# Optimization experiments

Hardware: AMD Instinct MI355X
Metric: run time of the kernel (lower is better)

Reference implementation:

```python
import jax, jax.numpy as jnp
import numpy as np

B = 256        # graph pairs
MAX_SET = 64   # nodes per graph == max_set_size (padding is identity)
E = 512        # edges per graph
D = 128        # node_state_dim == av.filters_3
T = 64         # av.transform_dim
N_PROP = 5
N_TIME = 3
TEMP = 0.1
SINK_ITERS = 20
NG = 2 * B
N = NG * MAX_SET
TOT_E = NG * E


def sinkhorn(log_alpha):
    la = log_alpha / TEMP
    for _ in range(SINK_ITERS):
        la = la - jax.nn.logsumexp(la, axis=2, keepdims=True)
        la = la - jax.nn.logsumexp(la, axis=1, keepdims=True)
    return jnp.exp(la)


def setup_inputs() -> dict:
    key = jax.random.key(0)
    ks = jax.random.split(key, 32)

    def lin(k, i, o):
        return jax.random.normal(k, (i, o), jnp.float32) / np.sqrt(i).astype(np.float32)

    node_features = jax.random.normal(ks[0], (N, 32), jnp.float32)
    edge_features = jax.random.normal(ks[1], (TOT_E, 16), jnp.float32)
    offs = jnp.repeat(jnp.arange(NG, dtype=jnp.int32) * MAX_SET, E)
    from_idx = jax.random.randint(ks[2], (TOT_E,), 0, MAX_SET, jnp.int32) + offs
    to_idx = jax.random.randint(ks[3], (TOT_E,), 0, MAX_SET, jnp.int32) + offs
    return {
        "node_features": node_features, "edge_features": edge_features,
        "from_idx": from_idx, "to_idx": to_idx,
        "node_enc_w": lin(ks[4], 32, D), "node_enc_b": jnp.zeros((D,), jnp.float32),
        "edge_enc_w": lin(ks[5], 16, 64), "edge_enc_b": jnp.zeros((64,), jnp.float32),
        "mw1": lin(ks[6], 2 * D + 64, 2 * D), "mb1": jnp.zeros((2 * D,), jnp.float32),
        "mw2": lin(ks[7], 2 * D, D), "mb2": jnp.zeros((D,), jnp.float32),
        "nw1": lin(ks[8], 2 * D, 2 * D), "nb1": jnp.zeros((2 * D,), jnp.float32),
        "nw2": lin(ks[9], 2 * D, D), "nb2": jnp.zeros((D,), jnp.float32),
        "cw1": lin(ks[10], 2 * D, 2 * D), "cb1": jnp.zeros((2 * D,), jnp.float32),
        "cw2": lin(ks[11], 2 * D, D), "cb2": jnp.zeros((D,), jnp.float32),
        "t1w": lin(ks[12], D, T), "t1b": jnp.zeros((T,), jnp.float32),
        "t2w": lin(ks[13], T, T), "t2b": jnp.zeros((T,), jnp.float32),
    }


def reference(node_features, edge_features, from_idx, to_idx,
              node_enc_w, node_enc_b, edge_enc_w, edge_enc_b,
              mw1, mb1, mw2, mb2, nw1, nb1, nw2, nb2,
              cw1, cb1, cw2, cb2, t1w, t1b, t2w, t2b):
    # Encoder (GMN GraphEncoder: linear maps on raw node/edge features)
    h0 = node_features @ node_enc_w + node_enc_b          # [N, D]
    e0 = edge_features @ edge_enc_w + edge_enc_b          # [TOT_E, 64]
    store = jnp.zeros((N, D * (N_PROP + 1)), h0.dtype)    # node_feature_store
    plan = None
    for _t in range(N_TIME):
        h = h0
        parts = [jnp.zeros((N, D), h0.dtype)]             # slot 0 stays zero
        for p in range(1, N_PROP + 1):
            inter = store[:, (p - 1) * D: p * D]          # time_update_idx == 'k_t'
            comb = jax.nn.relu(jnp.concatenate([h, inter], 1) @ cw1 + cb1) @ cw2 + cb2
            # GraphPropLayer: gather -> message MLP -> segment_sum -> node update MLP
            msg_in = jnp.concatenate([comb[from_idx], comb[to_idx], e0], 1)
            messages = jax.nn.relu(msg_in @ mw1 + mb1) @ mw2 + mb2
            agg = jax.ops.segment_sum(messages, to_idx, num_segments=N)
            h = jax.nn.relu(jnp.concatenate([comb, agg], 1) @ nw1 + nb1) @ nw2 + nb2
            parts.append(h)
        store = jnp.concatenate(parts, 1)                 # [N, D*(K+1)]
        # split into padded query/corpus stacks (all graphs have MAX_SET nodes,
        # so F.pad and the size masks are identity here)
        s = store.reshape(NG, MAX_SET, -1)
        q, c = s[0::2], s[1::2]                           # [B, M, D*(K+1)]
        tq = jax.nn.relu(q[:, :, -D:] @ t1w + t1b) @ t2w + t2b
        tc = jax.nn.relu(c[:, :, -D:] @ t1w + t1b) @ t2w + t2b
        sim = jnp.einsum('bqt,bct->bqc', tq, tc)
        plan = sinkhorn(sim)                              # node transport plan [B,M,M]
        qfc = jnp.einsum('bqc,bcd->bqd', plan, c)
        cfq = jnp.einsum('bqc,bqd->bcd', plan, q)
        inter_feats = jnp.stack([qfc, cfq], 1)[:, :, :, D:].reshape(N, N_PROP * D)
        store = store.at[:, D:].set(inter_feats)
    return plan
```

## Files before the change

### kernel.cpp

```cpp
#include <hip/hip_runtime.h>
#include <hip/hip_bf16.h>

#define NNODES   32768
#define NGROUPS  512
#define EPG      512
#define ND       (32768l*128)

typedef __attribute__((ext_vector_type(4))) float f32x4;
typedef __attribute__((ext_vector_type(8))) short bf16x8;

__device__ __forceinline__ short f2bf(float x) {
  unsigned u = __float_as_uint(x);
  unsigned r = (u + 0x7FFF + ((u >> 16) & 1)) >> 16;
  return (short)r;
}
__device__ __forceinline__ float bf2f(short h) {
  return __uint_as_float(((unsigned)(unsigned short)h) << 16);
}
__device__ __forceinline__ void split3(float x, short* ph, short* pm, short* pl, int idx) {
  short h = f2bf(x); float r1 = x - bf2f(h);
  short m = f2bf(r1); float r2 = r1 - bf2f(m);
  ph[idx] = h; pm[idx] = m; pl[idx] = f2bf(r2);
}

__global__ void k_node_enc(const float* __restrict__ nf, const float* __restrict__ w,
                           const float* __restrict__ b, float* __restrict__ h0) {
  int idx = blockIdx.x * 256 + threadIdx.x;
  int row = idx >> 7, col = idx & 127;
  const float* x = nf + row * 32;
  float acc = b[col];
#pragma unroll
  for (int k = 0; k < 32; ++k) acc = fmaf(x[k], w[k * 128 + col], acc);
  h0[idx] = acc;
}

__global__ void k_prep(const float* __restrict__ eew, const float* __restrict__ eeb,
                       const float* __restrict__ mw1, const float* __restrict__ mb1,
                       const float* __restrict__ mb2, const float* __restrict__ nw1,
                       float* __restrict__ Wfold, float* __restrict__ bfold,
                       float* __restrict__ vbias) {
  const int c = threadIdx.x, b = blockIdx.x;
  if (b < 16) {
    float a = 0.f;
    for (int j = 0; j < 64; ++j) a = fmaf(eew[b * 64 + j], mw1[(256 + j) * 256 + c], a);
    Wfold[b * 256 + c] = a;
  } else if (b == 16) {
    float a = mb1[c];
    for (int j = 0; j < 64; ++j) a = fmaf(eeb[j], mw1[(256 + j) * 256 + c], a);
    bfold[c] = a;
  } else {
    float a = 0.f;
    for (int j = 0; j < 128; ++j) a = fmaf(mb2[j], nw1[(128 + j) * 256 + c], a);
    vbias[c] = a;
  }
}

__global__ void k_wsplit3(const float* __restrict__ W, int C, int Kd,
                          short* __restrict__ th, short* __restrict__ tm,
                          short* __restrict__ tl) {
  const int c = blockIdx.x;
  for (int k = threadIdx.x; k < Kd; k += 256) {
    float w = W[(long)k * C + c];
    split3(w, th, tm, tl, c * 256 + k);
  }
}

__global__ void k_csr(const int* __restrict__ from_idx, const int* __restrict__ to_idx,
                      const float* __restrict__ ef,
                      int* __restrict__ csr_f, int* __restrict__ rp_g,
                      float* __restrict__ efp, int* __restrict__ deg) {
  __shared__ int cnt[64], rps[65];
  __shared__ int tls[EPG], fls[EPG];
  __shared__ short ord[EPG];
  const int g = blockIdx.x, tid = threadIdx.x;
  const int be = g * EPG, bn = g * 64;
  if (tid < 64) cnt[tid] = 0;
  __syncthreads();
  for (int e = tid; e < EPG; e += 256) {
    int t = to_idx[be + e] - bn;
    tls[e] = t;
    fls[e] = from_idx[be + e] - bn;
    atomicAdd(&cnt[t], 1);
  }
  __syncthreads();
  if (tid == 0) {
    int s = 0;
    for (int i = 0; i < 64; ++i) { rps[i] = s; s += cnt[i]; }
    rps[64] = s;
  }
  __syncthreads();
  if (tid < 64) {
    int pos = rps[tid];
    for (int e = 0; e < EPG; ++e)
      if (tls[e] == tid) ord[pos++] = (short)e;
  }
  __syncthreads();
  for (int ec = tid; ec < EPG; ec += 256) {
    const int eo = ord[ec];
    csr_f[be + ec] = fls[eo];
    const float4* src = (const float4*)&ef[(long)(be + eo) * 16];
    float4* dst = (float4*)&efp[(long)(be + ec) * 16];
    dst[0] = src[0]; dst[1] = src[1]; dst[2] = src[2]; dst[3] = src[3];
  }
  if (tid < 65) rp_g[g * 65 + tid] = rps[tid];
  if (tid < 64) deg[bn + tid] = cnt[tid];
}

template<int KTOT, bool DEG, bool SUM2>
__global__ __launch_bounds__(256, 2)
void k_mlp2m(const float* __restrict__ x0, const float* __restrict__ x1,
             const float* __restrict__ x1b,
             const short* __restrict__ W1h, const short* __restrict__ W1m,
             const short* __restrict__ W1l,
             const float* __restrict__ b1, const int* __restrict__ deg,
             const float* __restrict__ vbias,
             const short* __restrict__ W2h, const short* __restrict__ W2m,
             const short* __restrict__ W2l,
             const float* __restrict__ b2, float* __restrict__ out) {
  __shared__ short xh[32 * 264];
  __shared__ short xm[32 * 264];
  __shared__ short xl[32 * 264];
  __shared__ int degs[32];
  const int tid = threadIdx.x;
  const long row0 = (long)blockIdx.x * 32;

  for (int i = tid; i < 32 * 32; i += 256) {
    const int r = i >> 5, q = i & 31;
    float4 v = *(const float4*)&x0[(row0 + r) * 128 + q * 4];
    const int base = r * 264 + q * 4;
    split3(v.x, xh, xm, xl, base + 0);
    split3(v.y, xh, xm, xl, base + 1);
    split3(v.z, xh, xm, xl, base + 2);
    split3(v.w, xh, xm, xl, base + 3);
  }
  if constexpr (KTOT == 256) {
    for (int i = tid; i < 32 * 32; i += 256) {
      const int r = i >> 5, q = i & 31;
      float4 v = *(const float4*)&x1[(row0 + r) * 128 + q * 4];
      if constexpr (SUM2) {
        float4 w = *(const float4*)&x1b[(row0 + r) * 128 + q * 4];
        v.x += w.x; v.y += w.y; v.z += w.z; v.w += w.w;
      }
      const int base = r * 264 + 128 + q * 4;
      split3(v.x, xh, xm, xl, base + 0);
      split3(v.y, xh, xm, xl, base + 1);
      split3(v.z, xh, xm, xl, base + 2);
      split3(v.w, xh, xm, xl, base + 3);
    }
  }
  if constexpr (DEG) { if (tid < 32) degs[tid] = deg[row0 + tid]; }
  __syncthreads();

  const int lane = tid & 63, wid = tid >> 6;
  const int lr = lane & 15;
  const int lk = (lane >> 4) * 8;
  const int rsub = (lane >> 4) * 4;

  f32x4 acc[2][4];
#pragma unroll
  for (int fc = 0; fc < 4; ++fc) {
    const int col = wid * 64 + fc * 16 + lr;
    const float bv = b1[col];
#pragma unroll
    for (int fr = 0; fr < 2; ++fr) acc[fr][fc] = {bv, bv, bv, bv};
    if constexpr (DEG) {
      const float vb = vbias[col];
#pragma unroll
      for (int fr = 0; fr < 2; ++fr)
#pragma unroll
        for (int r = 0; r < 4; ++r)
          acc[fr][fc][r] += (float)degs[fr * 16 + rsub + r] * vb;
    }
  }

  for (int ks = 0; ks < KTOT / 32; ++ks) {
    const int k0 = ks * 32 + lk;
    bf16x8 ah[2], am[2], al[2];
#pragma unroll
    for (int fr = 0; fr < 2; ++fr) {
      const int ab = (fr * 16 + lr) * 264 + k0;
      ah[fr] = *(const bf16x8*)&xh[ab];
      am[fr] = *(const bf16x8*)&xm[ab];
      al[fr] = *(const bf16x8*)&xl[ab];
    }
#pragma unroll
    for (int fc = 0; fc < 4; ++fc) {
      const long wrow = (long)(wid * 64 + fc * 16 + lr) * 256 + k0;
      const bf16x8 bh = *(const bf16x8*)&W1h[wrow];
      const bf16x8 bm = *(const bf16x8*)&W1m[wrow];
      const bf16x8 bl = *(const bf16x8*)&W1l[wrow];
#pragma unroll
      for (int fr = 0; fr < 2; ++fr) {
        acc[fr][fc] = __builtin_amdgcn_mfma_f32_16x16x32_bf16(ah[fr], bh, acc[fr][fc], 0, 0, 0);
        acc[fr][fc] = __builtin_amdgcn_mfma_f32_16x16x32_bf16(ah[fr], bm, acc[fr][fc], 0, 0, 0);
        acc[fr][fc] = __builtin_amdgcn_mfma_f32_16x16x32_bf16(am[fr], bh, acc[fr][fc], 0, 0, 0);
        acc[fr][fc] = __builtin_amdgcn_mfma_f32_16x16x32_bf16(ah[fr], bl, acc[fr][fc], 0, 0, 0);
        acc[fr][fc] = __builtin_amdgcn_mfma_f32_16x16x32_bf16(am[fr], bm, acc[fr][fc], 0, 0, 0);
        acc[fr][fc] = __builtin_amdgcn_mfma_f32_16x16x32_bf16(al[fr], bh, acc[fr][fc], 0, 0, 0);
      }
    }
  }
  __syncthreads();

#pragma unroll
  for (int fr = 0; fr < 2; ++fr)
#pragma unroll
    for (int fc = 0; fc < 4; ++fc) {
      const int col = wid * 64 + fc * 16 + lr;
#pragma unroll
      for (int r = 0; r < 4; ++r) {
        const int row = fr * 16 + rsub + r;
        float v = fmaxf(acc[fr][fc][r], 0.f);
        split3(v, xh, xm, xl, row * 264 + col);
      }
    }
  __syncthreads();

  f32x4 acc2[2][2];
#pragma unroll
  for (int fc = 0; fc < 2; ++fc) {
    const float bv = b2[wid * 32 + fc * 16 + lr];
#pragma unroll
    for (int fr = 0; fr < 2; ++fr) acc2[fr][fc] = {bv, bv, bv, bv};
  }
  for (int ks = 0; ks < 8; ++ks) {
    const int k0 = ks * 32 + lk;
    bf16x8 ah[2], am[2], al[2];
#pragma unroll
    for (int fr = 0; fr < 2; ++fr) {
      const int ab = (fr * 16 + lr) * 264 + k0;
      ah[fr] = *(const bf16x8*)&xh[ab];
      am[fr] = *(const bf16x8*)&xm[ab];
      al[fr] = *(const bf16x8*)&xl[ab];
    }
#pragma unroll
    for (int fc = 0; fc < 2; ++fc) {
      const long wrow = (long)(wid * 32 + fc * 16 + lr) * 256 + k0;
      const bf16x8 bh = *(const bf16x8*)&W2h[wrow];
      const bf16x8 bm = *(const bf16x8*)&W2m[wrow];
      const bf16x8 bl = *(const bf16x8*)&W2l[wrow];
#pragma unroll
      for (int fr = 0; fr < 2; ++fr) {
        acc2[fr][fc] = __builtin_amdgcn_mfma_f32_16x16x32_bf16(ah[fr], bh, acc2[fr][fc], 0, 0, 0);
        acc2[fr][fc] = __builtin_amdgcn_mfma_f32_16x16x32_bf16(ah[fr], bm, acc2[fr][fc], 0, 0, 0);
        acc2[fr][fc] = __builtin_amdgcn_mfma_f32_16x16x32_bf16(am[fr], bh, acc2[fr][fc], 0, 0, 0);
        acc2[fr][fc] = __builtin_amdgcn_mfma_f32_16x16x32_bf16(ah[fr], bl, acc2[fr][fc], 0, 0, 0);
        acc2[fr][fc] = __builtin_amdgcn_mfma_f32_16x16x32_bf16(am[fr], bm, acc2[fr][fc], 0, 0, 0);
        acc2[fr][fc] = __builtin_amdgcn_mfma_f32_16x16x32_bf16(al[fr], bh, acc2[fr][fc], 0, 0, 0);
      }
    }
  }
#pragma unroll
  for (int fr = 0; fr < 2; ++fr)
#pragma unroll
    for (int fc = 0; fc < 2; ++fc) {
      const int col = wid * 32 + fc * 16 + lr;
#pragma unroll
      for (int r = 0; r < 4; ++r)
        out[(row0 + fr * 16 + rsub + r) * 128 + col] = acc2[fr][fc][r];
    }
}

__global__ __launch_bounds__(256, 3)
void k_edge(const float* __restrict__ comb, const float* __restrict__ efp,
            const float* __restrict__ mw1, const float* __restrict__ mw2,
            const float* __restrict__ Wfold, const float* __restrict__ bfold,
            const int* __restrict__ csr_f, const int* __restrict__ rp_g,
            float* __restrict__ aggM) {
  __shared__ __align__(16) float cA[64 * 64];
  __shared__ __align__(16) float U[128 * 64];
  __shared__ int fl[EPG];
  __shared__ int rp[65];
  float* ct = U;
  float* ag = U;

  const int tid = threadIdx.x;
  const int g = blockIdx.x, half = blockIdx.y;
  const int be = g * EPG, bn = g * 64;

  for (int i = tid; i < EPG; i += 256) fl[i] = csr_f[be + i];
  if (tid < 65) rp[tid] = rp_g[g * 65 + tid];

  const int ng = tid >> 4, cg = tid & 15;
  const int n0 = ng * 4, cq = cg * 4;

  float aM[4][8];
#pragma unroll
  for (int i = 0; i < 4; ++i)
#pragma unroll
    for (int j = 0; j < 8; ++j) aM[i][j] = 0.f;

  for (int cbi = 0; cbi < 2; ++cbi) {
    const int col0 = (half * 2 + cbi) * 64;
    __syncthreads();
    for (int i = tid; i < 2048; i += 256) {
      const int n = i & 63, q = i >> 6;
      float4 v = *(const float4*)&comb[(long)(bn + n) * 128 + q * 4];
      ct[(q*4+0)*64 + n] = v.x; ct[(q*4+1)*64 + n] = v.y;
      ct[(q*4+2)*64 + n] = v.z; ct[(q*4+3)*64 + n] = v.w;
    }
    __syncthreads();
    float accA[4][4], accB[4][4];
#pragma unroll
    for (int i = 0; i < 4; ++i)
#pragma unroll
      for (int j = 0; j < 4; ++j) { accA[i][j] = 0.f; accB[i][j] = 0.f; }
    {
      const int c0 = col0 + cq;
#pragma unroll 2
      for (int k = 0; k < 128; ++k) {
        const float4 xv = *(const float4*)&ct[k * 64 + n0];
        const float4 wa = *(const float4*)&mw1[k * 256 + c0];
        const float4 wb = *(const float4*)&mw1[(128 + k) * 256 + c0];
        const float xs_[4] = {xv.x, xv.y, xv.z, xv.w};
#pragma unroll
        for (int i = 0; i < 4; ++i) {
          accA[i][0] = fmaf(xs_[i], wa.x, accA[i][0]);
          accA[i][1] = fmaf(xs_[i], wa.y, accA[i][1]);
          accA[i][2] = fmaf(xs_[i], wa.z, accA[i][2]);
          accA[i][3] = fmaf(xs_[i], wa.w, accA[i][3]);
          accB[i][0] = fmaf(xs_[i], wb.x, accB[i][0]);
          accB[i][1] = fmaf(xs_[i], wb.y, accB[i][1]);
          accB[i][2] = fmaf(xs_[i], wb.z, accB[i][2]);
          accB[i][3] = fmaf(xs_[i], wb.w, accB[i][3]);
        }
      }
    }
    __syncthreads();
#pragma unroll
    for (int i = 0; i < 4; ++i)
      *(float4*)&cA[(n0 + i) * 64 + cq] =
        make_float4(accA[i][0], accA[i][1], accA[i][2], accA[i][3]);
    float4 Wf[16];
#pragma unroll
    for (int k = 0; k < 16; ++k) Wf[k] = *(const float4*)&Wfold[k * 256 + col0 + cq];
    const float4 bf = *(const float4*)&bfold[col0 + cq];
    __syncthreads();

#pragma unroll
    for (int i = 0; i < 4; ++i) {
      const int n = n0 + i;
      float4 acc = make_float4(0.f, 0.f, 0.f, 0.f);
      const float4 cB = make_float4(accB[i][0], accB[i][1], accB[i][2], accB[i][3]);
      const int e1 = rp[n + 1];
      for (int e = rp[n]; e < e1; ++e) {
        const int f = fl[e];
        const float* er = efp + (long)(be + e) * 16;
        float4 h = bf;
#pragma unroll
        for (int kq = 0; kq < 4; ++kq) {
          const float4 e4 = *(const float4*)(er + kq * 4);
          const float ev[4] = {e4.x, e4.y, e4.z, e4.w};
#pragma unroll
          for (int s = 0; s < 4; ++s) {
            const float4 w = Wf[kq * 4 + s];
            h.x = fmaf(ev[s], w.x, h.x); h.y = fmaf(ev[s], w.y, h.y);
            h.z = fmaf(ev[s], w.z, h.z); h.w = fmaf(ev[s], w.w, h.w);
          }
        }
        const float4 va = *(const float4*)&cA[f * 64 + cq];
        acc.x += fmaxf(h.x + va.x + cB.x, 0.f);
        acc.y += fmaxf(h.y + va.y + cB.y, 0.f);
        acc.z += fmaxf(h.z + va.z + cB.z, 0.f);
        acc.w += fmaxf(h.w + va.w + cB.w, 0.f);
      }
      *(float4*)&ag[n * 64 + cq] = acc;
    }
    __syncthreads();

    {
      const int c2 = cg * 8;
#pragma unroll 2
      for (int kk = 0; kk < 64; ++kk) {
        const float4 w0 = *(const float4*)&mw2[(col0 + kk) * 128 + c2];
        const float4 w1 = *(const float4*)&mw2[(col0 + kk) * 128 + c2 + 4];
#pragma unroll
        for (int i = 0; i < 4; ++i) {
          const float x = ag[(n0 + i) * 64 + kk];
          aM[i][0] = fmaf(x, w0.x, aM[i][0]); aM[i][1] = fmaf(x, w0.y, aM[i][1]);
          aM[i][2] = fmaf(x, w0.z, aM[i][2]); aM[i][3] = fmaf(x, w0.w, aM[i][3]);
          aM[i][4] = fmaf(x, w1.x, aM[i][4]); aM[i][5] = fmaf(x, w1.y, aM[i][5]);
          aM[i][6] = fmaf(x, w1.z, aM[i][6]); aM[i][7] = fmaf(x, w1.w, aM[i][7]);
        }
      }
    }
  }
  float* aggMh = aggM + (long)half * ND;
#pragma unroll
  for (int i = 0; i < 4; ++i) {
    *(float4*)&aggMh[(long)(bn + n0 + i) * 128 + cg * 8]     = *(float4*)&aM[i][0];
    *(float4*)&aggMh[(long)(bn + n0 + i) * 128 + cg * 8 + 4] = *(float4*)&aM[i][4];
  }
}

__global__ void k_tfeat(const float* __restrict__ x,
                        const float* __restrict__ t1w, const float* __restrict__ t1b,
                        const float* __restrict__ t2w, const float* __restrict__ t2b,
                        float* __restrict__ tf) {
  __shared__ float xs[4][128];
  __shared__ float ys[4][64];
  const int tid = threadIdx.x;
  const long row0 = (long)blockIdx.x * 4;
  for (int i = tid; i < 512; i += 256)
    xs[i >> 7][i & 127] = x[(row0 + (i >> 7)) * 128 + (i & 127)];
  __syncthreads();
  const int r = tid >> 6, c = tid & 63;
  float acc = t1b[c];
#pragma unroll 4
  for (int k = 0; k < 128; ++k) acc = fmaf(xs[r][k], t1w[k * 64 + c], acc);
  ys[r][c] = fmaxf(acc, 0.f);
  __syncthreads();
  float a2 = t2b[c];
#pragma unroll 4
  for (int k = 0; k < 64; ++k) a2 = fmaf(ys[r][k], t2w[k * 64 + c], a2);
  tf[(row0 + r) * 64 + c] = a2;
}

__global__ void k_sim(const float* __restrict__ tf, float* __restrict__ sim) {
  const int b = blockIdx.x, tid = threadIdx.x;
  __shared__ float tq[64][65];
  __shared__ float tcs[64][65];
  for (int i = tid; i < 4096; i += 256) {
    tq[i >> 6][i & 63]  = tf[(long)b * 8192 + i];
    tcs[i >> 6][i & 63] = tf[(long)b * 8192 + 4096 + i];
  }
  __syncthreads();
  const int m = tid >> 2, j0 = (tid & 3) * 16;
#pragma unroll
  for (int j = 0; j < 16; ++j) {
    float a = 0.f;
#pragma unroll 4
    for (int k = 0; k < 64; ++k) a = fmaf(tq[m][k], tcs[j0 + j][k], a);
    sim[(long)b * 4096 + m * 64 + j0 + j] = a;
  }
}

__global__ void k_sink(float* __restrict__ sim, float* __restrict__ outp) {
  const int b = blockIdx.x, tid = threadIdx.x;
  __shared__ float la[64][65];
  const float C = 14.426950408889634f;
  for (int i = tid; i < 4096; i += 256)
    la[i >> 6][i & 63] = sim[(long)b * 4096 + i] * C;
  __syncthreads();
  const int r4 = tid >> 2, l4 = tid & 3;
  for (int it = 0; it < 20; ++it) {
    {
      float m = -3.4e38f;
#pragma unroll
      for (int i = 0; i < 16; ++i) m = fmaxf(m, la[r4][l4 + 4 * i]);
      m = fmaxf(m, __shfl_xor(m, 1)); m = fmaxf(m, __shfl_xor(m, 2));
      float s = 0.f;
#pragma unroll
      for (int i = 0; i < 16; ++i) s += exp2f(la[r4][l4 + 4 * i] - m);
      s += __shfl_xor(s, 1); s += __shfl_xor(s, 2);
      const float lse = m + log2f(s);
#pragma unroll
      for (int i = 0; i < 16; ++i) la[r4][l4 + 4 * i] -= lse;
    }
    __syncthreads();
    {
      float m = -3.4e38f;
#pragma unroll
      for (int i = 0; i < 16; ++i) m = fmaxf(m, la[l4 + 4 * i][r4]);
      m = fmaxf(m, __shfl_xor(m, 1)); m = fmaxf(m, __shfl_xor(m, 2));
      float s = 0.f;
#pragma unroll
      for (int i = 0; i < 16; ++i) s += exp2f(la[l4 + 4 * i][r4] - m);
      s += __shfl_xor(s, 1); s += __shfl_xor(s, 2);
      const float lse = m + log2f(s);
#pragma unroll
      for (int i = 0; i < 16; ++i) la[l4 + 4 * i][r4] -= lse;
    }
    __syncthreads();
  }
  for (int i = tid; i < 4096; i += 256) {
    const float v = exp2f(la[i >> 6][i & 63]);
    outp[(long)b * 4096 + i] = v;
    sim[(long)b * 4096 + i] = v;
  }
}

__global__ void k_mix(const float* __restrict__ plan, const float* __restrict__ src,
                      float* __restrict__ dst) {
  const int b = blockIdx.x, tid = threadIdx.x;
  __shared__ float pl[64][65];
  __shared__ float qs[64][128];
  __shared__ float cs[64][128];
  const long qbase = (long)(2 * b) * 64, cbase = qbase + 64;
  for (int i = tid; i < 4096; i += 256) pl[i >> 6][i & 63] = plan[(long)b * 4096 + i];
  for (int i = tid; i < 8192; i += 256) {
    qs[i >> 7][i & 127] = src[qbase * 128 + i];
    cs[i >> 7][i & 127] = src[cbase * 128 + i];
  }
  __syncthreads();
  const int d = tid & 127, m0 = (tid >> 7) * 32;
  for (int m = m0; m < m0 + 32; ++m) {
    float a = 0.f;
#pragma unroll 4
    for (int j = 0; j < 64; ++j) a = fmaf(pl[m][j], cs[j][d], a);
    dst[(qbase + m) * 128 + d] = a;
  }
  for (int j = m0; j < m0 + 32; ++j) {
    float a = 0.f;
#pragma unroll 4
    for (int m = 0; m < 64; ++m) a = fmaf(pl[m][j], qs[m][d], a);
    dst[(cbase + j) * 128 + d] = a;
  }
}

extern "C" void kernel_launch(void* const* d_in, const int* in_sizes, int n_in,
                              void* d_out, int out_size, void* d_ws, size_t ws_size,
                              hipStream_t stream) {
  const float* nf  = (const float*)d_in[0];
  const float* ef  = (const float*)d_in[1];
  const int* from_idx = (const int*)d_in[2];
  const int* to_idx   = (const int*)d_in[3];
  const float* new_w = (const float*)d_in[4];
  const float* new_b = (const float*)d_in[5];
  const float* eew = (const float*)d_in[6];
  const float* eeb = (const float*)d_in[7];
  const float* mw1 = (const float*)d_in[8];
  const float* mb1 = (const float*)d_in[9];
  const float* mw2 = (const float*)d_in[10];
  const float* mb2 = (const float*)d_in[11];
  const float* nw1 = (const float*)d_in[12];
  const float* nb1 = (const float*)d_in[13];
  const float* nw2 = (const float*)d_in[14];
  const float* nb2 = (const float*)d_in[15];
  const float* cw1 = (const float*)d_in[16];
  const float* cb1 = (const float*)d_in[17];
  const float* cw2 = (const float*)d_in[18];
  const float* cb2 = (const float*)d_in[19];
  const float* t1w = (const float*)d_in[20];
  const float* t1b = (const float*)d_in[21];
  const float* t2w = (const float*)d_in[22];
  const float* t2b = (const float*)d_in[23];

  float* W = (float*)d_ws;
  float* h0     = W;
  float* comb   = h0 + ND;
  float* aggM0  = comb + ND;
  float* aggM1  = aggM0 + ND;
  float* parts  = aggM1 + ND;
  float* efp    = parts + 5 * ND;
  float* Wfold  = efp + 262144l * 16;
  float* bfold  = Wfold + 4096;
  float* vbias  = bfold + 256;
  int*   deg    = (int*)(vbias + 256);
  int*   csr_f  = deg + 32768;
  int*   rp_g   = csr_f + 262144;
  short* cw1t_h = (short*)(rp_g + 33280);
  short* cw1t_m = cw1t_h + 65536;
  short* cw1t_l = cw1t_m + 65536;
  short* nw1t_h = cw1t_l + 65536;
  short* nw1t_m = nw1t_h + 65536;
  short* nw1t_l = nw1t_m + 65536;
  short* cw2t_h = nw1t_l + 65536;
  short* cw2t_m = cw2t_h + 32768;
  short* cw2t_l = cw2t_m + 32768;
  short* nw2t_h = cw2t_l + 32768;
  short* nw2t_m = nw2t_h + 32768;
  short* nw2t_l = nw2t_m + 32768;
  float* tf     = aggM0;
  float* sim    = aggM0 + 2097152;
  float* outp   = (float*)d_out;

  k_prep<<<18, 256, 0, stream>>>(eew, eeb, mw1, mb1, mb2, nw1, Wfold, bfold, vbias);
  k_csr<<<512, 256, 0, stream>>>(from_idx, to_idx, ef, csr_f, rp_g, efp, deg);
  k_wsplit3<<<256, 256, 0, stream>>>(cw1, 256, 256, cw1t_h, cw1t_m, cw1t_l);
  k_wsplit3<<<256, 256, 0, stream>>>(nw1, 256, 256, nw1t_h, nw1t_m, nw1t_l);
  k_wsplit3<<<128, 256, 0, stream>>>(cw2, 128, 256, cw2t_h, cw2t_m, cw2t_l);
  k_wsplit3<<<128, 256, 0, stream>>>(nw2, 128, 256, nw2t_h, nw2t_m, nw2t_l);
  k_node_enc<<<16384, 256, 0, stream>>>(nf, new_w, new_b, h0);

  for (int t = 0; t < 3; ++t) {
    const float* hprev = h0;
    for (int p = 1; p <= 5; ++p) {
      if (t > 0 && p > 1)
        k_mlp2m<256, false, false><<<1024, 256, 0, stream>>>(
            hprev, parts + (long)(p - 1) * ND, nullptr,
            cw1t_h, cw1t_m, cw1t_l, cb1, nullptr, nullptr,
            cw2t_h, cw2t_m, cw2t_l, cb2, comb);
      else
        k_mlp2m<128, false, false><<<1024, 256, 0, stream>>>(
            hprev, nullptr, nullptr,
            cw1t_h, cw1t_m, cw1t_l, cb1, nullptr, nullptr,
            cw2t_h, cw2t_m, cw2t_l, cb2, comb);
      k_edge<<<dim3(512, 2), 256, 0, stream>>>(comb, efp, mw1, mw2, Wfold, bfold,
                                               csr_f, rp_g, aggM0);
      float* hnew = parts + (long)(p - 1) * ND;
      k_mlp2m<256, true, true><<<1024, 256, 0, stream>>>(
          comb, aggM0, aggM1,
          nw1t_h, nw1t_m, nw1t_l, nb1, deg, vbias,
          nw2t_h, nw2t_m, nw2t_l, nb2, hnew);
      hprev = hnew;
    }
    k_tfeat<<<8192, 256, 0, stream>>>(parts + 4 * ND, t1w, t1b, t2w, t2b, tf);
    k_sim<<<256, 256, 0, stream>>>(tf, sim);
    k_sink<<<256, 256, 0, stream>>>(sim, outp);
    if (t < 2) {
      for (int pi = 3; pi >= 0; --pi)
        k_mix<<<256, 256, 0, stream>>>(sim, parts + (long)pi * ND, parts + (long)(pi + 1) * ND);
    }
  }
}
```

Before: 6.685 ms.

## Move edge-message GEMMs onto split-bf16 MFMA and store comb pre-split

The edge kernel's two dense projections (comb times mw1 halves, and aggregated hidden times mw2) were scalar fp32 FMA loops. They now use 3-way bf16-split MFMA matching the node MLP kernels, with mw1 and mw2 pre-split once. The comb-producing MLP now writes its output already split into hi/mid/lo bf16 planes, so both the edge kernel and the node-update MLP load them directly instead of re-splitting. This trades fp32 SIMD work for matrix-core work plus extra global traffic from three bf16 planes. Occupancy also drops from 3 to 2 blocks per CU because of the larger LDS footprint.

```diff
diff --git a/kernel.cpp b/kernel.cpp
--- a/kernel.cpp
+++ b/kernel.cpp
@@ -17,7 +17,7 @@
 __device__ __forceinline__ float bf2f(short h) {
   return __uint_as_float(((unsigned)(unsigned short)h) << 16);
 }
-__device__ __forceinline__ void split3(float x, short* ph, short* pm, short* pl, int idx) {
+__device__ __forceinline__ void split3(float x, short* ph, short* pm, short* pl, long idx) {
   short h = f2bf(x); float r1 = x - bf2f(h);
   short m = f2bf(r1); float r2 = r1 - bf2f(m);
   ph[idx] = h; pm[idx] = m; pl[idx] = f2bf(r2);
@@ -106,17 +106,22 @@
   if (tid < 64) deg[bn + tid] = cnt[tid];
 }
 
-template<int KTOT, bool DEG, bool SUM2>
+template<int KTOT, bool DEG, bool SUM2, bool RPX0, bool WPOUT>
 __global__ __launch_bounds__(256, 2)
-void k_mlp2m(const float* __restrict__ x0, const float* __restrict__ x1,
-             const float* __restrict__ x1b,
+void k_mlp2m(const float* __restrict__ x0,
+             const short* __restrict__ x0h, const short* __restrict__ x0m,
+             const short* __restrict__ x0l,
+             const float* __restrict__ x1, const float* __restrict__ x1b,
              const short* __restrict__ W1h, const short* __restrict__ W1m,
              const short* __restrict__ W1l,
              const float* __restrict__ b1, const int* __restrict__ deg,
              const float* __restrict__ vbias,
              const short* __restrict__ W2h, const short* __restrict__ W2m,
              const short* __restrict__ W2l,
-             const float* __restrict__ b2, float* __restrict__ out) {
+             const float* __restrict__ b2,
+             float* __restrict__ out,
+             short* __restrict__ outh, short* __restrict__ outm,
+             short* __restrict__ outl) {
   __shared__ short xh[32 * 264];
   __shared__ short xm[32 * 264];
   __shared__ short xl[32 * 264];
@@ -124,14 +129,25 @@
   const int tid = threadIdx.x;
   const long row0 = (long)blockIdx.x * 32;
 
-  for (int i = tid; i < 32 * 32; i += 256) {
-    const int r = i >> 5, q = i & 31;
-    float4 v = *(const float4*)&x0[(row0 + r) * 128 + q * 4];
-    const int base = r * 264 + q * 4;
-    split3(v.x, xh, xm, xl, base + 0);
-    split3(v.y, xh, xm, xl, base + 1);
-    split3(v.z, xh, xm, xl, base + 2);
-    split3(v.w, xh, xm, xl, base + 3);
+  if constexpr (RPX0) {
+    for (int i = tid; i < 32 * 16; i += 256) {
+      const int r = i >> 4, q = i & 15;
+      const long gb = (row0 + r) * 128 + q * 8;
+      const int lb = r * 264 + q * 8;
+      *(bf16x8*)&xh[lb] = *(const bf16x8*)&x0h[gb];
+      *(bf16x8*)&xm[lb] = *(const bf16x8*)&x0m[gb];
+      *(bf16x8*)&xl[lb] = *(const bf16x8*)&x0l[gb];
+    }
+  } else {
+    for (int i = tid; i < 32 * 32; i += 256) {
+      const int r = i >> 5, q = i & 31;
+      float4 v = *(const float4*)&x0[(row0 + r) * 128 + q * 4];
+      const int base = r * 264 + q * 4;
+      split3(v.x, xh, xm, xl, base + 0);
+      split3(v.y, xh, xm, xl, base + 1);
+      split3(v.z, xh, xm, xl, base + 2);
+      split3(v.w, xh, xm, xl, base + 3);
+    }
   }
   if constexpr (KTOT == 256) {
     for (int i = tid; i < 32 * 32; i += 256) {
@@ -256,23 +272,35 @@
     for (int fc = 0; fc < 2; ++fc) {
       const int col = wid * 32 + fc * 16 + lr;
 #pragma unroll
-      for (int r = 0; r < 4; ++r)
-        out[(row0 + fr * 16 + rsub + r) * 128 + col] = acc2[fr][fc][r];
-    }
-}
-
-__global__ __launch_bounds__(256, 3)
-void k_edge(const float* __restrict__ comb, const float* __restrict__ efp,
-            const float* __restrict__ mw1, const float* __restrict__ mw2,
-            const float* __restrict__ Wfold, const float* __restrict__ bfold,
-            const int* __restrict__ csr_f, const int* __restrict__ rp_g,
-            float* __restrict__ aggM) {
-  __shared__ __align__(16) float cA[64 * 64];
-  __shared__ __align__(16) float U[128 * 64];
+      for (int r = 0; r < 4; ++r) {
+        const long gi = (row0 + fr * 16 + rsub + r) * 128 + col;
+        if constexpr (WPOUT) {
+          split3(acc2[fr][fc][r], outh, outm, outl, gi);
+        } else {
+          out[gi] = acc2[fr][fc][r];
+        }
+      }
+    }
+}
+
+__global__ __launch_bounds__(256, 2)
+void k_edgem(const short* __restrict__ chp, const short* __restrict__ cmp,
+             const short* __restrict__ clp,
+             const float* __restrict__ efp,
+             const short* __restrict__ m1h, const short* __restrict__ m1m,
+             const short* __restrict__ m1l,
+             const short* __restrict__ m2h, const short* __restrict__ m2m,
+             const short* __restrict__ m2l,
+             const float* __restrict__ Wfold, const float* __restrict__ bfold,
+             const int* __restrict__ csr_f, const int* __restrict__ rp_g,
+             float* __restrict__ aggM) {
+  __shared__ __align__(16) float cAB[2 * 64 * 68];
+  __shared__ __align__(16) float ag[64 * 68];
   __shared__ int fl[EPG];
   __shared__ int rp[65];
-  float* ct = U;
-  float* ag = U;
+  float* cA = cAB;
+  float* cB = cAB + 64 * 68;
+  short* agp = (short*)cAB;
 
   const int tid = threadIdx.x;
   const int g = blockIdx.x, half = blockIdx.y;
@@ -281,56 +309,70 @@
   for (int i = tid; i < EPG; i += 256) fl[i] = csr_f[be + i];
   if (tid < 65) rp[tid] = rp_g[g * 65 + tid];
 
+  const int lane = tid & 63, wid = tid >> 6;
+  const int lr = lane & 15;
+  const int lk = (lane >> 4) * 8;
+  const int rsub = (lane >> 4) * 4;
   const int ng = tid >> 4, cg = tid & 15;
   const int n0 = ng * 4, cq = cg * 4;
 
-  float aM[4][8];
-#pragma unroll
-  for (int i = 0; i < 4; ++i)
-#pragma unroll
-    for (int j = 0; j < 8; ++j) aM[i][j] = 0.f;
+  f32x4 aM[4][2];
+#pragma unroll
+  for (int fr = 0; fr < 4; ++fr)
+#pragma unroll
+    for (int fc = 0; fc < 2; ++fc) aM[fr][fc] = {0.f, 0.f, 0.f, 0.f};
 
   for (int cbi = 0; cbi < 2; ++cbi) {
     const int col0 = (half * 2 + cbi) * 64;
     __syncthreads();
-    for (int i = tid; i < 2048; i += 256) {
-      const int n = i & 63, q = i >> 6;
-      float4 v = *(const float4*)&comb[(long)(bn + n) * 128 + q * 4];
-      ct[(q*4+0)*64 + n] = v.x; ct[(q*4+1)*64 + n] = v.y;
-      ct[(q*4+2)*64 + n] = v.z; ct[(q*4+3)*64 + n] = v.w;
-    }
-    __syncthreads();
-    float accA[4][4], accB[4][4];
-#pragma unroll
-    for (int i = 0; i < 4; ++i)
-#pragma unroll
-      for (int j = 0; j < 4; ++j) { accA[i][j] = 0.f; accB[i][j] = 0.f; }
+
     {
-      const int c0 = col0 + cq;
-#pragma unroll 2
-      for (int k = 0; k < 128; ++k) {
-        const float4 xv = *(const float4*)&ct[k * 64 + n0];
-        const float4 wa = *(const float4*)&mw1[k * 256 + c0];
-        const float4 wb = *(const float4*)&mw1[(128 + k) * 256 + c0];
-        const float xs_[4] = {xv.x, xv.y, xv.z, xv.w};
-#pragma unroll
-        for (int i = 0; i < 4; ++i) {
-          accA[i][0] = fmaf(xs_[i], wa.x, accA[i][0]);
-          accA[i][1] = fmaf(xs_[i], wa.y, accA[i][1]);
-          accA[i][2] = fmaf(xs_[i], wa.z, accA[i][2]);
-          accA[i][3] = fmaf(xs_[i], wa.w, accA[i][3]);
-          accB[i][0] = fmaf(xs_[i], wb.x, accB[i][0]);
-          accB[i][1] = fmaf(xs_[i], wb.y, accB[i][1]);
-          accB[i][2] = fmaf(xs_[i], wb.z, accB[i][2]);
-          accB[i][3] = fmaf(xs_[i], wb.w, accB[i][3]);
+      const int isB = wid >> 1;
+      const int cw = (wid & 1) * 32;
+      const int wkof = isB * 128;
+      f32x4 c[4][2];
+#pragma unroll
+      for (int fr = 0; fr < 4; ++fr)
+#pragma unroll
+        for (int fc = 0; fc < 2; ++fc) c[fr][fc] = {0.f, 0.f, 0.f, 0.f};
+      for (int ks = 0; ks < 4; ++ks) {
+        const int k0 = ks * 32 + lk;
+        bf16x8 ah[4], am[4], al[4];
+#pragma unroll
+        for (int fr = 0; fr < 4; ++fr) {
+          const long ga = (long)(bn + fr * 16 + lr) * 128 + k0;
+          ah[fr] = *(const bf16x8*)&chp[ga];
+          am[fr] = *(const bf16x8*)&cmp[ga];
+          al[fr] = *(const bf16x8*)&clp[ga];
         }
-      }
-    }
-    __syncthreads();
-#pragma unroll
-    for (int i = 0; i < 4; ++i)
-      *(float4*)&cA[(n0 + i) * 64 + cq] =
-        make_float4(accA[i][0], accA[i][1], accA[i][2], accA[i][3]);
+#pragma unroll
+        for (int fc = 0; fc < 2; ++fc) {
+          const long wrow = (long)(col0 + cw + fc * 16 + lr) * 256 + wkof + k0;
+          const bf16x8 bh = *(const bf16x8*)&m1h[wrow];
+          const bf16x8 bm = *(const bf16x8*)&m1m[wrow];
+          const bf16x8 bl = *(const bf16x8*)&m1l[wrow];
+#pragma unroll
+          for (int fr = 0; fr < 4; ++fr) {
+            c[fr][fc] = __builtin_amdgcn_mfma_f32_16x16x32_bf16(ah[fr], bh, c[fr][fc], 0, 0, 0);
+            c[fr][fc] = __builtin_amdgcn_mfma_f32_16x16x32_bf16(ah[fr], bm, c[fr][fc], 0, 0, 0);
+            c[fr][fc] = __builtin_amdgcn_mfma_f32_16x16x32_bf16(am[fr], bh, c[fr][fc], 0, 0, 0);
+            c[fr][fc] = __builtin_amdgcn_mfma_f32_16x16x32_bf16(ah[fr], bl, c[fr][fc], 0, 0, 0);
+            c[fr][fc] = __builtin_amdgcn_mfma_f32_16x16x32_bf16(am[fr], bm, c[fr][fc], 0, 0, 0);
+            c[fr][fc] = __builtin_amdgcn_mfma_f32_16x16x32_bf16(al[fr], bh, c[fr][fc], 0, 0, 0);
+          }
+        }
+      }
+      float* dstC = isB ? cB : cA;
+#pragma unroll
+      for (int fr = 0; fr < 4; ++fr)
+#pragma unroll
+        for (int fc = 0; fc < 2; ++fc) {
+          const int col = cw + fc * 16 + lr;
+#pragma unroll
+          for (int r = 0; r < 4; ++r)
+            dstC[(fr * 16 + rsub + r) * 68 + col] = c[fr][fc][r];
+        }
+    }
     float4 Wf[16];
 #pragma unroll
     for (int k = 0; k < 16; ++k) Wf[k] = *(const float4*)&Wfold[k * 256 + col0 + cq];
@@ -341,7 +383,7 @@
     for (int i = 0; i < 4; ++i) {
       const int n = n0 + i;
       float4 acc = make_float4(0.f, 0.f, 0.f, 0.f);
-      const float4 cB = make_float4(accB[i][0], accB[i][1], accB[i][2], accB[i][3]);
+      const float4 cBn = *(const float4*)&cB[n * 68 + cq];
       const int e1 = rp[n + 1];
       for (int e = rp[n]; e < e1; ++e) {
         const int f = fl[e];
@@ -358,39 +400,66 @@
             h.z = fmaf(ev[s], w.z, h.z); h.w = fmaf(ev[s], w.w, h.w);
           }
         }
-        const float4 va = *(const float4*)&cA[f * 64 + cq];
-        acc.x += fmaxf(h.x + va.x + cB.x, 0.f);
-        acc.y += fmaxf(h.y + va.y + cB.y, 0.f);
-        acc.z += fmaxf(h.z + va.z + cB.z, 0.f);
-        acc.w += fmaxf(h.w + va.w + cB.w, 0.f);
-      }
-      *(float4*)&ag[n * 64 + cq] = acc;
+        const float4 va = *(const float4*)&cA[f * 68 + cq];
+        acc.x += fmaxf(h.x + va.x + cBn.x, 0.f);
+        acc.y += fmaxf(h.y + va.y + cBn.y, 0.f);
+        acc.z += fmaxf(h.z + va.z + cBn.z, 0.f);
+        acc.w += fmaxf(h.w + va.w + cBn.w, 0.f);
+      }
+      *(float4*)&ag[n * 68 + cq] = acc;
     }
     __syncthreads();
 
-    {
-      const int c2 = cg * 8;
-#pragma unroll 2
-      for (int kk = 0; kk < 64; ++kk) {
-        const float4 w0 = *(const float4*)&mw2[(col0 + kk) * 128 + c2];
-        const float4 w1 = *(const float4*)&mw2[(col0 + kk) * 128 + c2 + 4];
-#pragma unroll
-        for (int i = 0; i < 4; ++i) {
-          const float x = ag[(n0 + i) * 64 + kk];
-          aM[i][0] = fmaf(x, w0.x, aM[i][0]); aM[i][1] = fmaf(x, w0.y, aM[i][1]);
-          aM[i][2] = fmaf(x, w0.z, aM[i][2]); aM[i][3] = fmaf(x, w0.w, aM[i][3]);
-          aM[i][4] = fmaf(x, w1.x, aM[i][4]); aM[i][5] = fmaf(x, w1.y, aM[i][5]);
-          aM[i][6] = fmaf(x, w1.z, aM[i][6]); aM[i][7] = fmaf(x, w1.w, aM[i][7]);
+    for (int i = tid; i < 1024; i += 256) {
+      const int n = i >> 4, kq = (i & 15) * 4;
+      const float4 v = *(const float4*)&ag[n * 68 + kq];
+      const int b0 = n * 72 + kq;
+      split3(v.x, agp, agp + 4608, agp + 9216, b0 + 0);
+      split3(v.y, agp, agp + 4608, agp + 9216, b0 + 1);
+      split3(v.z, agp, agp + 4608, agp + 9216, b0 + 2);
+      split3(v.w, agp, agp + 4608, agp + 9216, b0 + 3);
+    }
+    __syncthreads();
+
+    for (int ks = 0; ks < 2; ++ks) {
+      const int k0 = ks * 32 + lk;
+      bf16x8 ah[4], am[4], al[4];
+#pragma unroll
+      for (int fr = 0; fr < 4; ++fr) {
+        const int ab = (fr * 16 + lr) * 72 + k0;
+        ah[fr] = *(const bf16x8*)&agp[ab];
+        am[fr] = *(const bf16x8*)&agp[4608 + ab];
+        al[fr] = *(const bf16x8*)&agp[9216 + ab];
+      }
+#pragma unroll
+      for (int fc = 0; fc < 2; ++fc) {
+        const long wrow = (long)(wid * 32 + fc * 16 + lr) * 256 + col0 + k0;
+        const bf16x8 bh = *(const bf16x8*)&m2h[wrow];
+        const bf16x8 bm = *(const bf16x8*)&m2m[wrow];
+        const bf16x8 bl = *(const bf16x8*)&m2l[wrow];
+#pragma unroll
+        for (int fr = 0; fr < 4; ++fr) {
+          aM[fr][fc] = __builtin_amdgcn_mfma_f32_16x16x32_bf16(ah[fr], bh, aM[fr][fc], 0, 0, 0);
+          aM[fr][fc] = __builtin_amdgcn_mfma_f32_16x16x32_bf16(ah[fr], bm, aM[fr][fc], 0, 0, 0);
+          aM[fr][fc] = __builtin_amdgcn_mfma_f32_16x16x32_bf16(am[fr], bh, aM[fr][fc], 0, 0, 0);
+          aM[fr][fc] = __builtin_amdgcn_mfma_f32_16x16x32_bf16(ah[fr], bl, aM[fr][fc], 0, 0, 0);
+          aM[fr][fc] = __builtin_amdgcn_mfma_f32_16x16x32_bf16(am[fr], bm, aM[fr][fc], 0, 0, 0);
+          aM[fr][fc] = __builtin_amdgcn_mfma_f32_16x16x32_bf16(al[fr], bh, aM[fr][fc], 0, 0, 0);
         }
       }
     }
   }
+
   float* aggMh = aggM + (long)half * ND;
 #pragma unroll
-  for (int i = 0; i < 4; ++i) {
-    *(float4*)&aggMh[(long)(bn + n0 + i) * 128 + cg * 8]     = *(float4*)&aM[i][0];
-    *(float4*)&aggMh[(long)(bn + n0 + i) * 128 + cg * 8 + 4] = *(float4*)&aM[i][4];
-  }
+  for (int fr = 0; fr < 4; ++fr)
+#pragma unroll
+    for (int fc = 0; fc < 2; ++fc) {
+      const int col = wid * 32 + fc * 16 + lr;
+#pragma unroll
+      for (int r = 0; r < 4; ++r)
+        aggMh[(long)(bn + fr * 16 + rsub + r) * 128 + col] = aM[fr][fc][r];
+    }
 }
 
 __global__ void k_tfeat(const float* __restrict__ x,
@@ -538,8 +607,7 @@
 
   float* W = (float*)d_ws;
   float* h0     = W;
-  float* comb   = h0 + ND;
-  float* aggM0  = comb + ND;
+  float* aggM0  = h0 + ND;
   float* aggM1  = aggM0 + ND;
   float* parts  = aggM1 + ND;
   float* efp    = parts + 5 * ND;
@@ -561,6 +629,15 @@
   short* nw2t_h = cw2t_l + 32768;
   short* nw2t_m = nw2t_h + 32768;
   short* nw2t_l = nw2t_m + 32768;
+  short* m1t_h  = nw2t_l + 32768;
+  short* m1t_m  = m1t_h + 65536;
+  short* m1t_l  = m1t_m + 65536;
+  short* m2t_h  = m1t_l + 65536;
+  short* m2t_m  = m2t_h + 32768;
+  short* m2t_l  = m2t_m + 32768;
+  short* chp    = m2t_l + 32768;
+  short* cmp    = chp + 32768l * 128;
+  short* clp    = cmp + 32768l * 128;
   float* tf     = aggM0;
   float* sim    = aggM0 + 2097152;
   float* outp   = (float*)d_out;
@@ -571,28 +648,33 @@
   k_wsplit3<<<256, 256, 0, stream>>>(nw1, 256, 256, nw1t_h, nw1t_m, nw1t_l);
   k_wsplit3<<<128, 256, 0, stream>>>(cw2, 128, 256, cw2t_h, cw2t_m, cw2t_l);
   k_wsplit3<<<128, 256, 0, stream>>>(nw2, 128, 256, nw2t_h, nw2t_m, nw2t_l);
+  k_wsplit3<<<256, 256, 0, stream>>>(mw1, 256, 256, m1t_h, m1t_m, m1t_l);
+  k_wsplit3<<<128, 256, 0, stream>>>(mw2, 128, 256, m2t_h, m2t_m, m2t_l);
   k_node_enc<<<16384, 256, 0, stream>>>(nf, new_w, new_b, h0);
 
   for (int t = 0; t < 3; ++t) {
     const float* hprev = h0;
     for (int p = 1; p <= 5; ++p) {
       if (t > 0 && p > 1)
-        k_mlp2m<256, false, false><<<1024, 256, 0, stream>>>(
-            hprev, parts + (long)(p - 1) * ND, nullptr,
+        k_mlp2m<256, false, false, false, true><<<1024, 256, 0, stream>>>(
+            hprev, nullptr, nullptr, nullptr,
+            parts + (long)(p - 1) * ND, nullptr,
             cw1t_h, cw1t_m, cw1t_l, cb1, nullptr, nullptr,
-            cw2t_h, cw2t_m, cw2t_l, cb2, comb);
+            cw2t_h, cw2t_m, cw2t_l, cb2, nullptr, chp, cmp, clp);
       else
-        k_mlp2m<128, false, false><<<1024, 256, 0, stream>>>(
-            hprev, nullptr, nullptr,
+        k_mlp2m<128, false, false, false, true><<<1024, 256, 0, stream>>>(
+            hprev, nullptr, nullptr, nullptr, nullptr, nullptr,
             cw1t_h, cw1t_m, cw1t_l, cb1, nullptr, nullptr,
-            cw2t_h, cw2t_m, cw2t_l, cb2, comb);
-      k_edge<<<dim3(512, 2), 256, 0, stream>>>(comb, efp, mw1, mw2, Wfold, bfold,
-                                               csr_f, rp_g, aggM0);
+            cw2t_h, cw2t_m, cw2t_l, cb2, nullptr, chp, cmp, clp);
+      k_edgem<<<dim3(512, 2), 256, 0, stream>>>(chp, cmp, clp, efp,
+                                                m1t_h, m1t_m, m1t_l,
+                                                m2t_h, m2t_m, m2t_l,
+                                                Wfold, bfold, csr_f, rp_g, aggM0);
       float* hnew = parts + (long)(p - 1) * ND;
-      k_mlp2m<256, true, true><<<1024, 256, 0, stream>>>(
-          comb, aggM0, aggM1,
+      k_mlp2m<256, true, true, true, false><<<1024, 256, 0, stream>>>(
+          nullptr, chp, cmp, clp, aggM0, aggM1,
           nw1t_h, nw1t_m, nw1t_l, nb1, deg, vbias,
-          nw2t_h, nw2t_m, nw2t_l, nb2, hnew);
+          nw2t_h, nw2t_m, nw2t_l, nb2, hnew, nullptr, nullptr, nullptr);
       hprev = hnew;
     }
     k_tfeat<<<8192, 256, 0, stream>>>(parts + 4 * ND, t1w, t1b, t2w, t2b, tf);
```

After: 6.441 ms. 3.7% less time.
